# Kernel tuning notes

Hardware: AMD Instinct MI355X
Metric: run time of the kernel (lower is better)

The kernel has to match this reference:

```python
import jax, jax.numpy as jnp
import numpy as np

DIM = 1024; HEADS = 16; HEAD_DIM = 64; LAYERS = 6
P = 2; IMG = 64; CIN = 4; NUM_CLASSES = 1000
CONV_C = DIM // 2  # 512
FF = 2816  # multiple_of-rounded int(2*4*DIM/3)
GN_GROUPS = 32
BATCH = 4


def _layernorm(x, g=None, b=None, eps=1e-5):
    mu = x.mean(-1, keepdims=True)
    var = x.var(-1, keepdims=True)
    xn = (x - mu) / jnp.sqrt(var + eps)
    if g is not None:
        xn = xn * g + b
    return xn


def _groupnorm(x, g, b, eps=1e-5):
    Bn, C, H, W = x.shape
    xr = x.reshape(Bn, GN_GROUPS, C // GN_GROUPS, H, W)
    mu = xr.mean((2, 3, 4), keepdims=True)
    var = xr.var((2, 3, 4), keepdims=True)
    xn = ((xr - mu) / jnp.sqrt(var + eps)).reshape(Bn, C, H, W)
    return xn * g[None, :, None, None] + b[None, :, None, None]


def _conv(x, w, b):
    y = jax.lax.conv_general_dilated(x, w, (1, 1), 'SAME',
                                     dimension_numbers=('NCHW', 'OIHW', 'NCHW'))
    return y + b[None, :, None, None]


def _freqs(T):
    inv = 1.0 / (10000.0 ** (jnp.arange(0, HEAD_DIM, 2, dtype=jnp.float32) / HEAD_DIM))
    f = jnp.arange(T, dtype=jnp.float32)[:, None] * inv[None, :]
    return jnp.stack([jnp.cos(f), jnp.sin(f)], axis=-1)  # [T, HEAD_DIM//2, 2]


def _rope(x, fc):
    # x: [B, T, H, D]; fc: [T, D//2, 2]
    xr = x.reshape(*x.shape[:-1], -1, 2)
    x0, x1 = xr[..., 0], xr[..., 1]
    f0 = fc[None, :, None, :, 0]
    f1 = fc[None, :, None, :, 1]
    y = jnp.stack([x0 * f0 - x1 * f1, x0 * f1 + x1 * f0], axis=-1)
    return y.reshape(x.shape)


def _modulate(x, shift, scale):
    return x * (1.0 + scale[:, None, :]) + shift[:, None, :]


def _forward(x, t, conv1_w, conv1_b, gn1_g, gn1_b, conv2_w, conv2_b, gn2_g, gn2_b,
             xemb_w, xemb_b, t1_w, t1_b, t2_w, t2_b, y_emb,
             wq, wk, wv, wo, w1, w2, w3, ada_w, ada_b, an_g, an_b, fn_g, fn_b,
             fin_ada_w, fin_ada_b, fin_w, fin_b, y):
    # init conv stack: Conv-SiLU-GN x2
    h = _conv(x, conv1_w, conv1_b)
    h = _groupnorm(jax.nn.silu(h), gn1_g, gn1_b)
    h = _conv(h, conv2_w, conv2_b)
    h = _groupnorm(jax.nn.silu(h), gn2_g, gn2_b)
    # patchify: [B,C,H,W] -> [B, N, C*P*P]
    Bn, C, H, W = h.shape
    hp, wp = H // P, W // P
    h = h.reshape(Bn, C, hp, P, wp, P).transpose(0, 2, 4, 1, 3, 5).reshape(Bn, hp * wp, C * P * P)
    z = h @ xemb_w.T + xemb_b  # [B, N, DIM]
    # conditioning: timestep MLP + class embedding
    temb = t.reshape(-1, 1) @ t1_w.T + t1_b
    temb = jax.nn.silu(temb) @ t2_w.T + t2_b
    c = temb + y_emb[y]  # [B, DIM]
    c_silu = jax.nn.silu(c)
    T = z.shape[1]
    fc = _freqs(T)
    scale = HEAD_DIM ** -0.5
    for i in range(LAYERS):
        mods = c_silu @ ada_w[i].T + ada_b[i]
        sm, scm, gm, sp, scp, gp = jnp.split(mods, 6, axis=1)
        hh = _modulate(_layernorm(z, an_g[i], an_b[i]), sm, scm)
        q = (hh @ wq[i].T).reshape(Bn, T, HEADS, HEAD_DIM)
        k = (hh @ wk[i].T).reshape(Bn, T, HEADS, HEAD_DIM)
        v = (hh @ wv[i].T).reshape(Bn, T, HEADS, HEAD_DIM)
        q = _rope(q, fc)
        k = _rope(k, fc)
        scores = jnp.einsum('bthd,bshd->bhts', q, k) * scale
        attn = jax.nn.softmax(scores, axis=-1)
        out = jnp.einsum('bhts,bshd->bthd', attn, v).reshape(Bn, T, DIM)
        z = z + gm[:, None, :] * (out @ wo[i].T)
        hf = _modulate(_layernorm(z, fn_g[i], fn_b[i]), sp, scp)
        ff = (jax.nn.silu(hf @ w1[i].T) * (hf @ w3[i].T)) @ w2[i].T
        z = z + gp[:, None, :] * ff
    # final layer (norm has no affine, eps=1e-6)
    fm = c_silu @ fin_ada_w.T + fin_ada_b
    fs, fsc = jnp.split(fm, 2, axis=1)
    zf = _modulate(_layernorm(z, eps=1e-6), fs, fsc)
    o = zf @ fin_w.T + fin_b  # [B, N, P*P*CIN]
    # unpatchify -> [B, CIN, IMG, IMG]
    o = o.reshape(Bn, hp, wp, P, P, CIN).transpose(0, 5, 1, 3, 2, 4).reshape(Bn, CIN, hp * P, wp * P)
    return o


def setup_inputs() -> dict:
    ks = iter(jax.random.split(jax.random.key(0), 64))

    def nrm(shape, s=0.02):
        return jax.random.normal(next(ks), shape, jnp.float32) * s

    inp = {
        'x': jax.random.normal(next(ks), (BATCH, CIN, IMG, IMG), jnp.float32),
        't': jax.random.uniform(next(ks), (BATCH,), jnp.float32),
        'y': jax.random.randint(next(ks), (BATCH,), 0, NUM_CLASSES + 1),
        'conv1_w': nrm((CONV_C, CIN, 5, 5)), 'conv1_b': jnp.zeros((CONV_C,), jnp.float32),
        'gn1_g': jnp.ones((CONV_C,), jnp.float32), 'gn1_b': jnp.zeros((CONV_C,), jnp.float32),
        'conv2_w': nrm((CONV_C, CONV_C, 5, 5)), 'conv2_b': jnp.zeros((CONV_C,), jnp.float32),
        'gn2_g': jnp.ones((CONV_C,), jnp.float32), 'gn2_b': jnp.zeros((CONV_C,), jnp.float32),
        'xemb_w': nrm((DIM, P * P * CONV_C)), 'xemb_b': jnp.zeros((DIM,), jnp.float32),
        't1_w': nrm((DIM, 1)), 't1_b': jnp.zeros((DIM,), jnp.float32),
        't2_w': nrm((DIM, DIM)), 't2_b': jnp.zeros((DIM,), jnp.float32),
        'y_emb': nrm((NUM_CLASSES + 1, DIM)),
        'wq': nrm((LAYERS, DIM, DIM)), 'wk': nrm((LAYERS, DIM, DIM)),
        'wv': nrm((LAYERS, DIM, DIM)), 'wo': nrm((LAYERS, DIM, DIM)),
        'w1': nrm((LAYERS, FF, DIM)), 'w3': nrm((LAYERS, FF, DIM)), 'w2': nrm((LAYERS, DIM, FF)),
        'ada_w': nrm((LAYERS, 6 * DIM, DIM)), 'ada_b': jnp.zeros((LAYERS, 6 * DIM), jnp.float32),
        'an_g': jnp.ones((LAYERS, DIM), jnp.float32), 'an_b': jnp.zeros((LAYERS, DIM), jnp.float32),
        'fn_g': jnp.ones((LAYERS, DIM), jnp.float32), 'fn_b': jnp.zeros((LAYERS, DIM), jnp.float32),
        'fin_ada_w': nrm((2 * DIM, DIM)), 'fin_ada_b': jnp.zeros((2 * DIM,), jnp.float32),
        'fin_w': nrm((P * P * CIN, DIM)), 'fin_b': jnp.zeros((P * P * CIN,), jnp.float32),
    }
    return inp


def reference(x, t, y, conv1_w, conv1_b, gn1_g, gn1_b, conv2_w, conv2_b, gn2_g, gn2_b,
              xemb_w, xemb_b, t1_w, t1_b, t2_w, t2_b, y_emb,
              wq, wk, wv, wo, w1, w2, w3, ada_w, ada_b, an_g, an_b, fn_g, fn_b,
              fin_ada_w, fin_ada_b, fin_w, fin_b):
    return _forward(x, t, conv1_w, conv1_b, gn1_g, gn1_b, conv2_w, conv2_b, gn2_g, gn2_b,
                    xemb_w, xemb_b, t1_w, t1_b, t2_w, t2_b, y_emb,
                    wq, wk, wv, wo, w1, w2, w3, ada_w, ada_b, an_g, an_b, fn_g, fn_b,
                    fin_ada_w, fin_ada_b, fin_w, fin_b, y)
```

## Files before the change

### kernel.cpp

```cpp
#include <hip/hip_runtime.h>
#include <math.h>

#define NLAYERS 6

typedef unsigned short u16;
typedef unsigned int u32;
typedef __attribute__((ext_vector_type(4))) float floatx4;
typedef __attribute__((ext_vector_type(8))) short bf16x8;

__device__ __forceinline__ float silu_f(float x) { return x / (1.0f + __expf(-x)); }

__device__ __forceinline__ u16 f2b(float f) {
    union { float f; u32 u; } x; x.f = f;
    u32 r = x.u + 0x7fffu + ((x.u >> 16) & 1u);
    return (u16)(r >> 16);
}
__device__ __forceinline__ float b2f(u16 u) {
    union { u32 u; float f; } x; x.u = ((u32)u) << 16;
    return x.f;
}

__device__ __forceinline__ void gload_lds16(const void* g, void* l) {
    __builtin_amdgcn_global_load_lds((const __attribute__((address_space(1))) u32*)g,
                                     (__attribute__((address_space(3))) u32*)l, 16, 0, 0);
}

__device__ __forceinline__ void stage128x32(const u16* __restrict__ src, int ldk, short* lds, int t) {
    int w = t >> 6;
#pragma unroll
    for (int rep = 0; rep < 2; rep++) {
        int s = rep * 256 + t;
        int row = s >> 2, kp = s & 3;
        const u16* g = src + (size_t)row * ldk + kp * 8;
        short* lb = lds + (size_t)(rep * 256 + w * 64) * 8;
        gload_lds16((const void*)g, (void*)lb);
    }
}

__device__ __forceinline__ void stage_attn128x64(const u16* __restrict__ base, short* lds, int t) {
    int w = t >> 6;
#pragma unroll
    for (int rep = 0; rep < 4; rep++) {
        int cid = rep * 256 + t;
        int row = cid >> 3, cc = cid & 7;
        int gcc = cc ^ (row & 7);
        const u16* g = base + (size_t)row * 1024 + gcc * 8;
        short* lb = lds + (size_t)(rep * 256 + w * 64) * 8;
        gload_lds16((const void*)g, (void*)lb);
    }
}

__device__ __forceinline__ void stage_attn64x128(const u16* __restrict__ base, short* lds, int t) {
    int w = t >> 6;
#pragma unroll
    for (int rep = 0; rep < 4; rep++) {
        int cid = rep * 256 + t;
        int row = cid >> 4, cc = cid & 15;
        int gcc = (cc & 8) | ((cc ^ row) & 7);
        const u16* g = base + (size_t)row * 1024 + gcc * 8;
        short* lb = lds + (size_t)(rep * 256 + w * 64) * 8;
        gload_lds16((const void*)g, (void*)lb);
    }
}

__global__ __launch_bounds__(256) void mfma_gemm_kernel(
    const u16* __restrict__ A, const u16* __restrict__ W, int M, int N, int K,
    float* __restrict__ outF, u16* __restrict__ outB, const float* __restrict__ bias,
    float* __restrict__ accZ, const float* __restrict__ gate, int gateStride) {
    __shared__ __align__(16) short As[128 * 32];
    __shared__ __align__(16) short Bs[128 * 32];
    int t = threadIdx.x;
    int lane = t & 63, wave = t >> 6;
    int wm = wave >> 1, wn = wave & 1;
    int m0 = blockIdx.y << 7, n0 = blockIdx.x << 7;
    int lm = lane & 15, kg = lane >> 4;
    floatx4 zero4 = {0.f, 0.f, 0.f, 0.f};
    floatx4 acc[4][4];
#pragma unroll
    for (int i = 0; i < 4; i++)
#pragma unroll
        for (int j = 0; j < 4; j++) acc[i][j] = zero4;
    const u16* Arow = A + (size_t)m0 * K;
    const u16* Wrow = W + (size_t)n0 * K;
    int aoff[4], boff[4];
#pragma unroll
    for (int i = 0; i < 4; i++) {
        aoff[i] = (wm * 64 + i * 16 + lm) * 32 + kg * 8;
        boff[i] = (wn * 64 + i * 16 + lm) * 32 + kg * 8;
    }
    for (int k0 = 0; k0 < K; k0 += 32) {
        stage128x32(Arow + k0, K, As, t);
        stage128x32(Wrow + k0, K, Bs, t);
        __syncthreads();
        bf16x8 af[4], bfr[4];
#pragma unroll
        for (int i = 0; i < 4; i++) af[i] = *(const bf16x8*)&As[aoff[i]];
#pragma unroll
        for (int j = 0; j < 4; j++) bfr[j] = *(const bf16x8*)&Bs[boff[j]];
#pragma unroll
        for (int i = 0; i < 4; i++)
#pragma unroll
            for (int j = 0; j < 4; j++)
                acc[i][j] = __builtin_amdgcn_mfma_f32_16x16x32_bf16(af[i], bfr[j], acc[i][j], 0, 0, 0);
        __syncthreads();
    }
#pragma unroll
    for (int i = 0; i < 4; i++) {
        int rbase = m0 + wm * 64 + i * 16 + kg * 4;
#pragma unroll
        for (int j = 0; j < 4; j++) {
            int c = n0 + wn * 64 + j * 16 + lm;
#pragma unroll
            for (int r = 0; r < 4; r++) {
                float v = acc[i][j][r];
                int row = rbase + r;
                size_t off = (size_t)row * N + c;
                if (accZ) {
                    accZ[off] += gate[(row >> 10) * gateStride + c] * v;
                } else if (outB) {
                    outB[off] = f2b(v);
                } else {
                    if (bias) v += bias[c];
                    outF[off] = v;
                }
            }
        }
    }
}

__global__ __launch_bounds__(256) void mfma_gemm_swiglu_kernel(
    const u16* __restrict__ A, const u16* __restrict__ W1, const u16* __restrict__ W3,
    int M, int N, int K, u16* __restrict__ outB) {
    __shared__ __align__(16) short As[128 * 32];
    __shared__ __align__(16) short B1s[128 * 32];
    __shared__ __align__(16) short B3s[128 * 32];
    int t = threadIdx.x;
    int lane = t & 63, wave = t >> 6;
    int wm = wave >> 1, wn = wave & 1;
    int m0 = blockIdx.y << 7, n0 = blockIdx.x << 7;
    int lm = lane & 15, kg = lane >> 4;
    floatx4 zero4 = {0.f, 0.f, 0.f, 0.f};
    floatx4 acc1[4][4], acc3[4][4];
#pragma unroll
    for (int i = 0; i < 4; i++)
#pragma unroll
        for (int j = 0; j < 4; j++) { acc1[i][j] = zero4; acc3[i][j] = zero4; }
    const u16* Arow = A + (size_t)m0 * K;
    const u16* W1row = W1 + (size_t)n0 * K;
    const u16* W3row = W3 + (size_t)n0 * K;
    int aoff[4], boff[4];
#pragma unroll
    for (int i = 0; i < 4; i++) {
        aoff[i] = (wm * 64 + i * 16 + lm) * 32 + kg * 8;
        boff[i] = (wn * 64 + i * 16 + lm) * 32 + kg * 8;
    }
    for (int k0 = 0; k0 < K; k0 += 32) {
        stage128x32(Arow + k0, K, As, t);
        stage128x32(W1row + k0, K, B1s, t);
        stage128x32(W3row + k0, K, B3s, t);
        __syncthreads();
        bf16x8 af[4], b1[4], b3[4];
#pragma unroll
        for (int i = 0; i < 4; i++) af[i] = *(const bf16x8*)&As[aoff[i]];
#pragma unroll
        for (int j = 0; j < 4; j++) { b1[j] = *(const bf16x8*)&B1s[boff[j]]; b3[j] = *(const bf16x8*)&B3s[boff[j]]; }
#pragma unroll
        for (int i = 0; i < 4; i++)
#pragma unroll
            for (int j = 0; j < 4; j++) {
                acc1[i][j] = __builtin_amdgcn_mfma_f32_16x16x32_bf16(af[i], b1[j], acc1[i][j], 0, 0, 0);
                acc3[i][j] = __builtin_amdgcn_mfma_f32_16x16x32_bf16(af[i], b3[j], acc3[i][j], 0, 0, 0);
            }
        __syncthreads();
    }
#pragma unroll
    for (int i = 0; i < 4; i++) {
        int rbase = m0 + wm * 64 + i * 16 + kg * 4;
#pragma unroll
        for (int j = 0; j < 4; j++) {
            int c = n0 + wn * 64 + j * 16 + lm;
#pragma unroll
            for (int r = 0; r < 4; r++) {
                int row = rbase + r;
                float v = silu_f(acc1[i][j][r]) * acc3[i][j][r];
                outB[(size_t)row * N + c] = f2b(v);
            }
        }
    }
}

__global__ void f2bN_kernel(const float* __restrict__ p0, const float* __restrict__ p1,
                            const float* __restrict__ p2, const float* __restrict__ p3,
                            u16* __restrict__ out, int n4each, int nptr) {
    int idx = blockIdx.x * 256 + threadIdx.x;
    if (idx >= n4each * nptr) return;
    int which = idx / n4each;
    int i = idx - which * n4each;
    const float* p = (which == 0) ? p0 : (which == 1) ? p1 : (which == 2) ? p2 : p3;
    float4 v = ((const float4*)p)[i];
    ushort4 o;
    o.x = f2b(v.x); o.y = f2b(v.y); o.z = f2b(v.z); o.w = f2b(v.w);
    ((ushort4*)out)[idx] = o;
}

__global__ void temb1_kernel(const float* __restrict__ t, const float* __restrict__ w,
                             const float* __restrict__ b, float* __restrict__ out) {
    int idx = blockIdx.x * 256 + threadIdx.x;
    int bb = idx >> 10, n = idx & 1023;
    out[idx] = silu_f(t[bb] * w[n] + b[n]);
}

__global__ __launch_bounds__(256) void temb2_kernel(const float* __restrict__ A, const float* __restrict__ W,
                                                    const float* __restrict__ b2, const float* __restrict__ yemb,
                                                    const int* __restrict__ y, float* __restrict__ out) {
    int wid = blockIdx.x * 4 + (threadIdx.x >> 6);
    int lane = threadIdx.x & 63;
    int bb = wid >> 10, n = wid & 1023;
    const float* a = A + (bb << 10);
    const float* w = W + (n << 10);
    float s = 0.f;
    for (int k = lane << 2; k < 1024; k += 256) {
        float4 av = *(const float4*)&a[k];
        float4 wv = *(const float4*)&w[k];
        s += av.x * wv.x + av.y * wv.y + av.z * wv.z + av.w * wv.w;
    }
#pragma unroll
    for (int off = 32; off > 0; off >>= 1) s += __shfl_xor(s, off);
    if (lane == 0) {
        float vv = s + b2[n] + yemb[(size_t)y[bb] * 1024 + n];
        out[wid] = silu_f(vv);
    }
}

__global__ __launch_bounds__(256) void conv1_kernel(const float* __restrict__ x, const float* __restrict__ w,
                                                    const float* __restrict__ bias, float* __restrict__ out) {
    int idx = blockIdx.x * 256 + threadIdx.x;
    int px = idx & 63;
    int py = (idx >> 6) & 63;
    int oc = (idx >> 12) & 511;
    int b = idx >> 21;
    float acc = bias[oc];
    for (int ic = 0; ic < 4; ic++) {
        const float* xp = x + (((b << 2) + ic) << 12);
        const float* wp = w + (oc * 4 + ic) * 25;
#pragma unroll
        for (int ky = 0; ky < 5; ky++) {
            int iy = py + ky - 2;
            if (iy < 0 || iy > 63) continue;
#pragma unroll
            for (int kx = 0; kx < 5; kx++) {
                int ix = px + kx - 2;
                if (ix < 0 || ix > 63) continue;
                acc += xp[(iy << 6) + ix] * wp[ky * 5 + kx];
            }
        }
    }
    out[idx] = acc;
}

__global__ __launch_bounds__(256) void silu_gn_kernel(const float* __restrict__ in, float* __restrict__ out,
                                                      const float* __restrict__ g, const float* __restrict__ bt) {
    int blk = blockIdx.x;
    int b = blk >> 5, grp = blk & 31, c0 = grp << 4;
    const float* p = in + (size_t)((b * 512 + c0)) * 4096;
    float* q = out + (size_t)((b * 512 + c0)) * 4096;
    int t = threadIdx.x;
    float s = 0.f, sq = 0.f;
    for (int i = t; i < 16384; i += 256) {
        float4 v = ((const float4*)p)[i];
        float a0 = silu_f(v.x), a1 = silu_f(v.y), a2 = silu_f(v.z), a3 = silu_f(v.w);
        s += a0 + a1 + a2 + a3;
        sq += a0 * a0 + a1 * a1 + a2 * a2 + a3 * a3;
    }
    __shared__ float2 red[256];
    red[t] = make_float2(s, sq);
    __syncthreads();
    for (int st = 128; st > 0; st >>= 1) {
        if (t < st) { red[t].x += red[t + st].x; red[t].y += red[t + st].y; }
        __syncthreads();
    }
    float mean = red[0].x * (1.f / 65536.f);
    float var = red[0].y * (1.f / 65536.f) - mean * mean;
    float rstd = rsqrtf(var + 1e-5f);
    for (int i = t; i < 16384; i += 256) {
        float4 v = ((const float4*)p)[i];
        int ch = c0 + (i >> 10);
        float gg = g[ch], bb = bt[ch];
        float4 o;
        o.x = (silu_f(v.x) - mean) * rstd * gg + bb;
        o.y = (silu_f(v.y) - mean) * rstd * gg + bb;
        o.z = (silu_f(v.z) - mean) * rstd * gg + bb;
        o.w = (silu_f(v.w) - mean) * rstd * gg + bb;
        ((float4*)q)[i] = o;
    }
}

__global__ __launch_bounds__(256) void nchw2nhwc_pad_kernel(const float* __restrict__ in, u16* __restrict__ out) {
    int blk = blockIdx.x;
    int ct = blk & 15;
    int yy = (blk >> 4) & 63;
    int b = blk >> 10;
    __shared__ float tile[32][65];
    int t = threadIdx.x;
    const float* ip = in + (((size_t)(b * 512 + (ct << 5))) << 12) + (yy << 6);
    for (int i = t; i < 2048; i += 256) {
        int cl = i >> 6, x = i & 63;
        tile[cl][x] = ip[((size_t)cl << 12) + x];
    }
    __syncthreads();
    u16* op = out + ((size_t)((b * 68 + yy + 2) * 68 + 2)) * 512 + (ct << 5);
    for (int i = t; i < 2048; i += 256) {
        int x = i >> 5, cl = i & 31;
        op[(size_t)x * 512 + cl] = f2b(tile[cl][x]);
    }
}

__global__ __launch_bounds__(256) void wtrans25_kernel(const float* __restrict__ w, u16* __restrict__ wt) {
    int idx = blockIdx.x * 256 + threadIdx.x;
    const float* p = w + (size_t)idx * 25;
#pragma unroll
    for (int tap = 0; tap < 25; tap++)
        wt[(size_t)tap * 262144 + idx] = f2b(p[tap]);
}

__global__ __launch_bounds__(256) void conv2_mfma_kernel(
    const u16* __restrict__ Ipad, const u16* __restrict__ Wt,
    const float* __restrict__ bias, float* __restrict__ out) {
    __shared__ __align__(16) short As[128 * 32];
    __shared__ __align__(16) short Bs[128 * 32];
    int t = threadIdx.x;
    int lane = t & 63, wave = t >> 6;
    int wm = wave >> 1, wn = wave & 1;
    int m0 = blockIdx.y << 7;
    int b = blockIdx.x >> 5;
    int y0 = (blockIdx.x & 31) << 1;
    int lm = lane & 15, kg = lane >> 4;
    floatx4 zero4 = {0.f, 0.f, 0.f, 0.f};
    floatx4 acc[4][4];
#pragma unroll
    for (int i = 0; i < 4; i++)
#pragma unroll
        for (int j = 0; j < 4; j++) acc[i][j] = zero4;
    int aoff[4], boff[4];
#pragma unroll
    for (int i = 0; i < 4; i++) {
        aoff[i] = (wm * 64 + i * 16 + lm) * 32 + kg * 8;
        boff[i] = (wn * 64 + i * 16 + lm) * 32 + kg * 8;
    }
    int s0 = t, s1 = 256 + t;
    int row0 = s0 >> 2, kp0 = s0 & 3;
    int row1 = s1 >> 2, kp1 = s1 & 3;
    int po0 = (row0 >> 6) * 68 + (row0 & 63);
    int po1 = (row1 >> 6) * 68 + (row1 & 63);
    short* lb0 = Bs + (size_t)(wave * 64) * 8;
    short* lb1 = Bs + (size_t)(256 + wave * 64) * 8;
    const u16* ibase = Ipad + ((size_t)(b * 68 + y0) * 68) * 512;
    int tap = 0;
    for (int ky = 0; ky < 5; ky++) {
        for (int kx = 0; kx < 5; kx++, tap++) {
            const u16* wsrc = Wt + (size_t)tap * 262144 + (size_t)m0 * 512;
            const u16* isrc = ibase + (size_t)(ky * 68 + kx) * 512;
            const u16* g0 = isrc + (size_t)po0 * 512 + kp0 * 8;
            const u16* g1 = isrc + (size_t)po1 * 512 + kp1 * 8;
            for (int k0 = 0; k0 < 512; k0 += 32) {
                stage128x32(wsrc + k0, 512, As, t);
                gload_lds16((const void*)(g0 + k0), (void*)lb0);
                gload_lds16((const void*)(g1 + k0), (void*)lb1);
                __syncthreads();
                bf16x8 af[4], bfr[4];
#pragma unroll
                for (int i = 0; i < 4; i++) af[i] = *(const bf16x8*)&As[aoff[i]];
#pragma unroll
                for (int j = 0; j < 4; j++) bfr[j] = *(const bf16x8*)&Bs[boff[j]];
#pragma unroll
                for (int i = 0; i < 4; i++)
#pragma unroll
                    for (int j = 0; j < 4; j++)
                        acc[i][j] = __builtin_amdgcn_mfma_f32_16x16x32_bf16(af[i], bfr[j], acc[i][j], 0, 0, 0);
                __syncthreads();
            }
        }
    }
#pragma unroll
    for (int i = 0; i < 4; i++) {
        int ocbase = m0 + wm * 64 + i * 16 + kg * 4;
#pragma unroll
        for (int j = 0; j < 4; j++) {
            int c = wn * 64 + j * 16 + lm;
            int py = y0 + (c >> 6), px = c & 63;
#pragma unroll
            for (int r = 0; r < 4; r++) {
                int oc = ocbase + r;
                out[((size_t)(b * 512 + oc) << 12) + (py << 6) + px] = acc[i][j][r] + bias[oc];
            }
        }
    }
}

__global__ void patchify_kernel(const float* __restrict__ hn, u16* __restrict__ pout) {
    int idx = blockIdx.x * 256 + threadIdx.x;
    int kf = idx & 2047;
    int tk = (idx >> 11) & 1023;
    int b = idx >> 21;
    int c = kf >> 2;
    int a = (kf >> 1) & 1;
    int b2 = kf & 1;
    int ph = tk >> 5, pw = tk & 31;
    pout[idx] = f2b(hn[(size_t)((b * 512 + c)) * 4096 + (((ph << 1) + a) << 6) + (pw << 1) + b2]);
}

template <typename OT>
__global__ __launch_bounds__(256) void ln_mod_kernel(const float* __restrict__ in, OT* __restrict__ out,
                                                     const float* __restrict__ g, const float* __restrict__ bt,
                                                     const float* __restrict__ shiftb, const float* __restrict__ scaleb,
                                                     int modStride, float eps) {
    int row = blockIdx.x;
    int b = row >> 10;
    int t = threadIdx.x;
    const float* p = in + ((size_t)row << 10);
    float4 x = ((const float4*)p)[t];
    float s = x.x + x.y + x.z + x.w;
    float sq = x.x * x.x + x.y * x.y + x.z * x.z + x.w * x.w;
    __shared__ float2 red[256];
    red[t] = make_float2(s, sq);
    __syncthreads();
    for (int st = 128; st > 0; st >>= 1) {
        if (t < st) { red[t].x += red[t + st].x; red[t].y += red[t + st].y; }
        __syncthreads();
    }
    float mean = red[0].x * (1.f / 1024.f);
    float var = red[0].y * (1.f / 1024.f) - mean * mean;
    float rstd = rsqrtf(var + eps);
    const float* sh = shiftb + b * modStride;
    const float* sc = scaleb + b * modStride;
    int c = t << 2;
    float o0, o1, o2, o3;
    {
        float xn = (x.x - mean) * rstd; if (g) xn = xn * g[c + 0] + bt[c + 0];
        o0 = xn * (1.f + sc[c + 0]) + sh[c + 0];
    }
    {
        float xn = (x.y - mean) * rstd; if (g) xn = xn * g[c + 1] + bt[c + 1];
        o1 = xn * (1.f + sc[c + 1]) + sh[c + 1];
    }
    {
        float xn = (x.z - mean) * rstd; if (g) xn = xn * g[c + 2] + bt[c + 2];
        o2 = xn * (1.f + sc[c + 2]) + sh[c + 2];
    }
    {
        float xn = (x.w - mean) * rstd; if (g) xn = xn * g[c + 3] + bt[c + 3];
        o3 = xn * (1.f + sc[c + 3]) + sh[c + 3];
    }
    if constexpr (sizeof(OT) == 4) {
        float4 o = make_float4(o0, o1, o2, o3);
        ((float4*)(out + ((size_t)row << 10)))[t] = o;
    } else {
        ushort4 o;
        o.x = f2b(o0); o.y = f2b(o1); o.z = f2b(o2); o.w = f2b(o3);
        ((ushort4*)(out + ((size_t)row << 10)))[t] = o;
    }
}

__global__ void rope_table_kernel(float* __restrict__ RT) {
    int idx = blockIdx.x * 256 + threadIdx.x;
    int j = idx & 31;
    int tt = idx >> 5;
    float inv = powf(10000.f, -(float)j * (1.f / 32.f));
    float ang = (float)tt * inv;
    ((float2*)RT)[idx] = make_float2(cosf(ang), sinf(ang));
}

__global__ void rope_kernel(u16* __restrict__ p, const float* __restrict__ RT) {
    int idx = blockIdx.x * 256 + threadIdx.x;
    int j = idx & 31;
    int tt = (idx >> 9) & 1023;
    float2 cssn = ((const float2*)RT)[(tt << 5) + j];
    float cs = cssn.x, sn = cssn.y;
    int h = (idx >> 5) & 15;
    int b = idx >> 19;
    size_t base = (size_t)(((b << 10) + tt)) * 1024 + (h << 6) + (j << 1);
    ushort2 v = *(ushort2*)&p[base];
    float x = b2f(v.x), yv = b2f(v.y);
    ushort2 o;
    o.x = f2b(x * cs - yv * sn);
    o.y = f2b(x * sn + yv * cs);
    *(ushort2*)&p[base] = o;
}

__global__ __launch_bounds__(256) void vtrans_kernel(const u16* __restrict__ v, u16* __restrict__ vT) {
    int st = blockIdx.x, h = blockIdx.y, b = blockIdx.z;
    int s0 = st << 6;
    __shared__ u16 tile[64][68];
    int t = threadIdx.x;
#pragma unroll
    for (int rep = 0; rep < 4; rep++) {
        int i = rep * 256 + t;
        int sl = i >> 4, d4 = (i & 15) << 2;
        *(ushort4*)&tile[sl][d4] =
            *(const ushort4*)&v[(size_t)((b << 10) + s0 + sl) * 1024 + (h << 6) + d4];
    }
    __syncthreads();
#pragma unroll
    for (int rep = 0; rep < 4; rep++) {
        int i = rep * 256 + t;
        int d = i >> 4, sl4 = (i & 15) << 2;
        ushort4 o;
        o.x = tile[sl4 + 0][d];
        o.y = tile[sl4 + 1][d];
        o.z = tile[sl4 + 2][d];
        o.w = tile[sl4 + 3][d];
        *(ushort4*)&vT[(size_t)(((b * 16 + h) << 6) + d) * 1024 + s0 + sl4] = o;
    }
}

__global__ __launch_bounds__(256, 2) void attn_mfma_kernel(
    const u16* __restrict__ q, const u16* __restrict__ k,
    const u16* __restrict__ vT, u16* __restrict__ o) {
    __shared__ __align__(16) short Ks[128 * 64];
    __shared__ __align__(16) short Vts[64 * 128];
    __shared__ __align__(16) short Ps[4 * 32 * 128];
    int t = threadIdx.x;
    int lane = t & 63, wm = t >> 6;
    int lm = lane & 15, kg = lane >> 4;
    int tq0 = blockIdx.x << 7, h = blockIdx.y, b = blockIdx.z;

    const u16* qbase = q + ((size_t)((b << 10) + tq0 + wm * 32)) * 1024 + (h << 6);
    bf16x8 afq[2][2];
#pragma unroll
    for (int i = 0; i < 2; i++)
#pragma unroll
        for (int kk = 0; kk < 2; kk++)
            afq[i][kk] = *(const bf16x8*)(qbase + (size_t)(i * 16 + lm) * 1024 + kk * 32 + kg * 8);

    floatx4 zero4 = {0.f, 0.f, 0.f, 0.f};
    floatx4 oacc[2][4];
    float m_[2][4], l_[2][4];
#pragma unroll
    for (int i = 0; i < 2; i++)
#pragma unroll
        for (int r = 0; r < 4; r++) { m_[i][r] = -3.0e38f; l_[i][r] = 0.f; }
#pragma unroll
    for (int i = 0; i < 2; i++)
#pragma unroll
        for (int jn = 0; jn < 4; jn++) oacc[i][jn] = zero4;

    const u16* kb0 = k + ((size_t)(b << 10)) * 1024 + (h << 6);
    const u16* vb0 = vT + ((size_t)((b * 16 + h) << 6)) * 1024;
    u16* Pw = (u16*)Ps + wm * 4096;

    for (int s0 = 0; s0 < 1024; s0 += 128) {
        stage_attn128x64(kb0 + (size_t)s0 * 1024, Ks, t);
        stage_attn64x128(vb0 + s0, Vts, t);
        __syncthreads();

        floatx4 sacc[2][8];
#pragma unroll
        for (int i = 0; i < 2; i++)
#pragma unroll
            for (int j = 0; j < 8; j++) sacc[i][j] = zero4;
#pragma unroll
        for (int j = 0; j < 8; j++) {
            int row = j * 16 + lm;
            bf16x8 bk0 = *(const bf16x8*)&Ks[row * 64 + ((kg ^ (row & 7)) << 3)];
            bf16x8 bk1 = *(const bf16x8*)&Ks[row * 64 + (((4 + kg) ^ (row & 7)) << 3)];
#pragma unroll
            for (int i = 0; i < 2; i++) {
                sacc[i][j] = __builtin_amdgcn_mfma_f32_16x16x32_bf16(afq[i][0], bk0, sacc[i][j], 0, 0, 0);
                sacc[i][j] = __builtin_amdgcn_mfma_f32_16x16x32_bf16(afq[i][1], bk1, sacc[i][j], 0, 0, 0);
            }
        }

        float al[2][4], ps[2][4];
#pragma unroll
        for (int i = 0; i < 2; i++)
#pragma unroll
            for (int r = 0; r < 4; r++) {
                float v = sacc[i][0][r];
#pragma unroll
                for (int j = 1; j < 8; j++) v = fmaxf(v, sacc[i][j][r]);
                v = fmaxf(v, __shfl_xor(v, 1));
                v = fmaxf(v, __shfl_xor(v, 2));
                v = fmaxf(v, __shfl_xor(v, 4));
                v = fmaxf(v, __shfl_xor(v, 8));
                float mn = fmaxf(m_[i][r], v * 0.125f);
                al[i][r] = __expf(m_[i][r] - mn);
                m_[i][r] = mn;
                l_[i][r] *= al[i][r];
                ps[i][r] = 0.f;
            }
#pragma unroll
        for (int i = 0; i < 2; i++)
#pragma unroll
            for (int jn = 0; jn < 4; jn++)
#pragma unroll
                for (int r = 0; r < 4; r++) oacc[i][jn][r] *= al[i][r];

#pragma unroll
        for (int i = 0; i < 2; i++)
#pragma unroll
            for (int j = 0; j < 8; j++) {
                int s = j * 16 + lm;
                int chunk = s >> 3;
#pragma unroll
                for (int r = 0; r < 4; r++) {
                    int qr = i * 16 + kg * 4 + r;
                    float e = __expf(fmaf(sacc[i][j][r], 0.125f, -m_[i][r]));
                    ps[i][r] += e;
                    int cs = (chunk & 8) | ((chunk ^ qr) & 7);
                    Pw[qr * 128 + cs * 8 + (s & 7)] = f2b(e);
                }
            }
#pragma unroll
        for (int i = 0; i < 2; i++)
#pragma unroll
            for (int r = 0; r < 4; r++) {
                float v = ps[i][r];
                v += __shfl_xor(v, 1);
                v += __shfl_xor(v, 2);
                v += __shfl_xor(v, 4);
                v += __shfl_xor(v, 8);
                l_[i][r] += v;
            }

#pragma unroll
        for (int ks = 0; ks < 4; ks++) {
            int chunk = ks * 4 + kg;
            bf16x8 pa[2];
#pragma unroll
            for (int i = 0; i < 2; i++) {
                int qr = i * 16 + lm;
                int cs = (chunk & 8) | ((chunk ^ qr) & 7);
                pa[i] = *(const bf16x8*)&Pw[qr * 128 + cs * 8];
            }
#pragma unroll
            for (int jn = 0; jn < 4; jn++) {
                int row = jn * 16 + lm;
                int cs = (chunk & 8) | ((chunk ^ row) & 7);
                bf16x8 bv = *(const bf16x8*)&Vts[row * 128 + cs * 8];
#pragma unroll
                for (int i = 0; i < 2; i++)
                    oacc[i][jn] = __builtin_amdgcn_mfma_f32_16x16x32_bf16(pa[i], bv, oacc[i][jn], 0, 0, 0);
            }
        }
        __syncthreads();
    }

    u16* obase = o + ((size_t)((b << 10) + tq0 + wm * 32)) * 1024 + (h << 6);
#pragma unroll
    for (int i = 0; i < 2; i++)
#pragma unroll
        for (int r = 0; r < 4; r++) {
            float inv = 1.f / l_[i][r];
            int qr = i * 16 + kg * 4 + r;
#pragma unroll
            for (int jn = 0; jn < 4; jn++)
                obase[(size_t)qr * 1024 + jn * 16 + lm] = f2b(oacc[i][jn][r] * inv);
        }
}

__global__ __launch_bounds__(256) void rowvec_gemm_kernel(const float* __restrict__ A, const float* __restrict__ W,
                                                          const float* __restrict__ bias, float* __restrict__ out,
                                                          int N, int K) {
    int wid = blockIdx.x * 4 + (threadIdx.x >> 6);
    int lane = threadIdx.x & 63;
    int b = wid / N, n = wid - b * N;
    const float* a = A + (size_t)b * K;
    const float* w = W + (size_t)n * K;
    float s = 0.f;
    for (int k = lane << 2; k < K; k += 256) {
        float4 av = *(const float4*)&a[k];
        float4 wv = *(const float4*)&w[k];
        s += av.x * wv.x + av.y * wv.y + av.z * wv.z + av.w * wv.w;
    }
#pragma unroll
    for (int off = 32; off > 0; off >>= 1) s += __shfl_xor(s, off);
    if (lane == 0) out[wid] = s + (bias ? bias[n] : 0.f);
}

__global__ __launch_bounds__(256) void fin_gemm_kernel(const float* __restrict__ zf, const float* __restrict__ w,
                                                       const float* __restrict__ bias, float* __restrict__ out) {
    int idx = blockIdx.x * 256 + threadIdx.x;
    int m = idx >> 4, n = idx & 15;
    const float* a = zf + ((size_t)m << 10);
    const float* wp = w + ((size_t)n << 10);
    float s = 0.f;
    for (int k = 0; k < 1024; k += 4) {
        float4 av = *(const float4*)&a[k];
        float4 wv = *(const float4*)&wp[k];
        s += av.x * wv.x + av.y * wv.y + av.z * wv.z + av.w * wv.w;
    }
    out[idx] = s + bias[n];
}

__global__ void unpatch_kernel(const float* __restrict__ ot, float* __restrict__ out) {
    int idx = blockIdx.x * 256 + threadIdx.x;
    int x = idx & 63;
    int yy = (idx >> 6) & 63;
    int ci = (idx >> 12) & 3;
    int b = idx >> 14;
    out[idx] = ot[(size_t)(((b << 10) + ((yy >> 1) << 5) + (x >> 1))) * 16 + (((yy & 1) << 1) + (x & 1)) * 4 + ci];
}

extern "C" void kernel_launch(void* const* d_in, const int* in_sizes, int n_in,
                              void* d_out, int out_size, void* d_ws, size_t ws_size,
                              hipStream_t stream) {
    const float* x       = (const float*)d_in[0];
    const float* tin     = (const float*)d_in[1];
    const int*   y       = (const int*)d_in[2];
    const float* conv1_w = (const float*)d_in[3];
    const float* conv1_b = (const float*)d_in[4];
    const float* gn1_g   = (const float*)d_in[5];
    const float* gn1_b   = (const float*)d_in[6];
    const float* conv2_w = (const float*)d_in[7];
    const float* conv2_b = (const float*)d_in[8];
    const float* gn2_g   = (const float*)d_in[9];
    const float* gn2_b   = (const float*)d_in[10];
    const float* xemb_w  = (const float*)d_in[11];
    const float* xemb_b  = (const float*)d_in[12];
    const float* t1_w    = (const float*)d_in[13];
    const float* t1_b    = (const float*)d_in[14];
    const float* t2_w    = (const float*)d_in[15];
    const float* t2_b    = (const float*)d_in[16];
    const float* y_emb   = (const float*)d_in[17];
    const float* wq      = (const float*)d_in[18];
    const float* wk      = (const float*)d_in[19];
    const float* wv      = (const float*)d_in[20];
    const float* wo      = (const float*)d_in[21];
    const float* w1      = (const float*)d_in[22];
    const float* w3      = (const float*)d_in[23];
    const float* w2      = (const float*)d_in[24];
    const float* ada_w   = (const float*)d_in[25];
    const float* ada_b   = (const float*)d_in[26];
    const float* an_g    = (const float*)d_in[27];
    const float* an_b    = (const float*)d_in[28];
    const float* fn_g    = (const float*)d_in[29];
    const float* fn_b    = (const float*)d_in[30];
    const float* fin_ada_w = (const float*)d_in[31];
    const float* fin_ada_b = (const float*)d_in[32];
    const float* fin_w   = (const float*)d_in[33];
    const float* fin_b   = (const float*)d_in[34];

    char* wsb = (char*)d_ws;
    float* Z    = (float*)(wsb + 0);
    u16*  Wbf   = (u16*)(wsb + (16ull << 20));
    u16*  HHb   = (u16*)(wsb + (34ull << 20));
    u16*  Qb    = (u16*)(wsb + (42ull << 20));
    u16*  Kb    = (u16*)(wsb + (50ull << 20));
    u16*  Vb    = (u16*)(wsb + (58ull << 20));
    u16*  VTb   = (u16*)(wsb + (66ull << 20));
    u16*  AOb   = (u16*)(wsb + (74ull << 20));
    u16*  F1b   = (u16*)(wsb + (82ull << 20));
    float* A0f  = (float*)(wsb + (42ull << 20));
    float* A1f  = (float*)(wsb + (76ull << 20));
    u16*  IPad  = (u16*)(wsb + 0);
    u16*  WTc   = (u16*)(wsb + (20ull << 20));
    u16*  PATb  = (u16*)(wsb + (16ull << 20));
    u16*  XWb   = (u16*)(wsb + (34ull << 20));
    float* ZF   = (float*)(wsb + (42ull << 20));
    float* SM   = (float*)(wsb + (110ull << 20));
    float* TMB  = SM;
    float* CSI  = TMB + 4096;
    float* MODS = CSI + 4096;
    float* FM   = MODS + 24576;
    float* OT   = FM + 8192;
    float* RT   = (float*)(wsb + (112ull << 20));

    hipMemsetAsync(IPad, 0, (size_t)4 * 68 * 68 * 512 * 2, stream);
    rope_table_kernel<<<128, 256, 0, stream>>>(RT);
    wtrans25_kernel<<<1024, 256, 0, stream>>>(conv2_w, WTc);

    temb1_kernel<<<16, 256, 0, stream>>>(tin, t1_w, t1_b, TMB);
    temb2_kernel<<<1024, 256, 0, stream>>>(TMB, t2_w, t2_b, y_emb, y, CSI);

    conv1_kernel<<<32768, 256, 0, stream>>>(x, conv1_w, conv1_b, A0f);
    silu_gn_kernel<<<128, 256, 0, stream>>>(A0f, A1f, gn1_g, gn1_b);
    nchw2nhwc_pad_kernel<<<4096, 256, 0, stream>>>(A1f, IPad);
    conv2_mfma_kernel<<<dim3(128, 4), 256, 0, stream>>>(IPad, WTc, conv2_b, A0f);
    silu_gn_kernel<<<128, 256, 0, stream>>>(A0f, A1f, gn2_g, gn2_b);
    patchify_kernel<<<32768, 256, 0, stream>>>(A1f, PATb);
    f2bN_kernel<<<2048, 256, 0, stream>>>(xemb_w, nullptr, nullptr, nullptr, XWb, 524288, 1);
    mfma_gemm_kernel<<<dim3(8, 32), 256, 0, stream>>>(PATb, XWb, 4096, 1024, 2048,
                                                      Z, nullptr, xemb_b, nullptr, nullptr, 0);

    for (int i = 0; i < NLAYERS; i++) {
        const float* wq_i = wq + (size_t)i * 1048576;
        const float* wk_i = wk + (size_t)i * 1048576;
        const float* wv_i = wv + (size_t)i * 1048576;
        const float* wo_i = wo + (size_t)i * 1048576;
        const float* w1_i = w1 + (size_t)i * 2883584;
        const float* w3_i = w3 + (size_t)i * 2883584;
        const float* w2_i = w2 + (size_t)i * 2883584;
        const float* ada_w_i = ada_w + (size_t)i * 6291456;
        const float* ada_b_i = ada_b + (size_t)i * 6144;

        f2bN_kernel<<<4096, 256, 0, stream>>>(wq_i, wk_i, wv_i, wo_i, Wbf, 262144, 4);
        rowvec_gemm_kernel<<<6144, 256, 0, stream>>>(CSI, ada_w_i, ada_b_i, MODS, 6144, 1024);
        ln_mod_kernel<u16><<<4096, 256, 0, stream>>>(Z, HHb, an_g + i * 1024, an_b + i * 1024,
                                                     MODS + 0, MODS + 1024, 6144, 1e-5f);
        mfma_gemm_kernel<<<dim3(8, 32), 256, 0, stream>>>(HHb, Wbf + 0ull, 4096, 1024, 1024,
                                                          nullptr, Qb, nullptr, nullptr, nullptr, 0);
        mfma_gemm_kernel<<<dim3(8, 32), 256, 0, stream>>>(HHb, Wbf + 1048576ull, 4096, 1024, 1024,
                                                          nullptr, Kb, nullptr, nullptr, nullptr, 0);
        mfma_gemm_kernel<<<dim3(8, 32), 256, 0, stream>>>(HHb, Wbf + 2097152ull, 4096, 1024, 1024,
                                                          nullptr, Vb, nullptr, nullptr, nullptr, 0);
        rope_kernel<<<8192, 256, 0, stream>>>(Qb, RT);
        rope_kernel<<<8192, 256, 0, stream>>>(Kb, RT);
        vtrans_kernel<<<dim3(16, 16, 4), 256, 0, stream>>>(Vb, VTb);
        attn_mfma_kernel<<<dim3(8, 16, 4), 256, 0, stream>>>(Qb, Kb, VTb, AOb);
        mfma_gemm_kernel<<<dim3(8, 32), 256, 0, stream>>>(AOb, Wbf + 3145728ull, 4096, 1024, 1024,
                                                          nullptr, nullptr, nullptr, Z, MODS + 2048, 6144);
        ln_mod_kernel<u16><<<4096, 256, 0, stream>>>(Z, HHb, fn_g + i * 1024, fn_b + i * 1024,
                                                     MODS + 3072, MODS + 4096, 6144, 1e-5f);
        f2bN_kernel<<<8448, 256, 0, stream>>>(w1_i, w3_i, w2_i, nullptr, Wbf, 720896, 3);
        mfma_gemm_swiglu_kernel<<<dim3(22, 32), 256, 0, stream>>>(HHb, Wbf, Wbf + 2883584ull,
                                                                  4096, 2816, 1024, F1b);
        mfma_gemm_kernel<<<dim3(8, 32), 256, 0, stream>>>(F1b, Wbf + 5767168ull, 4096, 1024, 2816,
                                                          nullptr, nullptr, nullptr, Z, MODS + 5120, 6144);
    }

    rowvec_gemm_kernel<<<2048, 256, 0, stream>>>(CSI, fin_ada_w, fin_ada_b, FM, 2048, 1024);
    ln_mod_kernel<float><<<4096, 256, 0, stream>>>(Z, ZF, nullptr, nullptr, FM + 0, FM + 1024, 2048, 1e-6f);
    fin_gemm_kernel<<<256, 256, 0, stream>>>(ZF, fin_w, fin_b, OT);
    unpatch_kernel<<<256, 256, 0, stream>>>(OT, (float*)d_out);
}
```

Measured before the change: 3.882 ms.

## Fuse QKV GEMMs with RoPE, add 128x64 GEMM tiles, prioritize attention MFMAs

Q, K and V projections now run as one GEMM over the concatenated weight (N=3072), and the epilogue applies RoPE using lane shuffles, so the three separate launches and two rope passes go away. N=1024 GEMMs (x-embed, output projection, FFN down) switch to a 128x64 tile kernel that launches 512 blocks instead of 256, which should fill the MI355X's many CUs better. The attention kernel raises wave priority with s_setprio around its MFMA loops. The trade-off is less reuse per block with the smaller tiles, and an extra RT table lookup in the QKV epilogue.

Result: faster. 3.463 ms (-10.8%).

```diff
diff --git a/kernel.cpp b/kernel.cpp
--- a/kernel.cpp
+++ b/kernel.cpp
@@ -35,6 +35,14 @@
         short* lb = lds + (size_t)(rep * 256 + w * 64) * 8;
         gload_lds16((const void*)g, (void*)lb);
     }
+}
+
+__device__ __forceinline__ void stage64x32(const u16* __restrict__ src, int ldk, short* lds, int t) {
+    int w = t >> 6;
+    int row = t >> 2, kp = t & 3;
+    const u16* g = src + (size_t)row * ldk + kp * 8;
+    short* lb = lds + (size_t)(w * 64) * 8;
+    gload_lds16((const void*)g, (void*)lb);
 }
 
 __device__ __forceinline__ void stage_attn128x64(const u16* __restrict__ base, short* lds, int t) {
@@ -63,10 +71,10 @@
     }
 }
 
-__global__ __launch_bounds__(256) void mfma_gemm_kernel(
-    const u16* __restrict__ A, const u16* __restrict__ W, int M, int N, int K,
-    float* __restrict__ outF, u16* __restrict__ outB, const float* __restrict__ bias,
-    float* __restrict__ accZ, const float* __restrict__ gate, int gateStride) {
+__global__ __launch_bounds__(256) void mfma_qkv_kernel(
+    const u16* __restrict__ A, const u16* __restrict__ W, const float* __restrict__ RT,
+    u16* __restrict__ Qb, u16* __restrict__ Kb, u16* __restrict__ Vb) {
+    const int K = 1024;
     __shared__ __align__(16) short As[128 * 32];
     __shared__ __align__(16) short Bs[128 * 32];
     int t = threadIdx.x;
@@ -110,6 +118,73 @@
 #pragma unroll
         for (int j = 0; j < 4; j++) {
             int c = n0 + wn * 64 + j * 16 + lm;
+            int which = c >> 10, cc = c & 1023;
+            u16* outp = (which == 0) ? Qb : (which == 1) ? Kb : Vb;
+            int fi = (cc >> 1) & 31;
+#pragma unroll
+            for (int r = 0; r < 4; r++) {
+                int row = rbase + r;
+                float v = acc[i][j][r];
+                float pv = __shfl_xor(v, 1);
+                float res = v;
+                if (which < 2) {
+                    int tt = row & 1023;
+                    float2 cssn = ((const float2*)RT)[(tt << 5) + fi];
+                    res = (lane & 1) ? fmaf(pv, cssn.y, v * cssn.x)
+                                     : fmaf(v, cssn.x, -pv * cssn.y);
+                }
+                outp[(size_t)row * 1024 + cc] = f2b(res);
+            }
+        }
+    }
+}
+
+__global__ __launch_bounds__(256) void mfma_gemm64_kernel(
+    const u16* __restrict__ A, const u16* __restrict__ W, int M, int N, int K,
+    float* __restrict__ outF, const float* __restrict__ bias,
+    float* __restrict__ accZ, const float* __restrict__ gate, int gateStride) {
+    __shared__ __align__(16) short As[128 * 32];
+    __shared__ __align__(16) short Bs[64 * 32];
+    int t = threadIdx.x;
+    int lane = t & 63, wave = t >> 6;
+    int wm = wave >> 1, wn = wave & 1;
+    int m0 = blockIdx.y << 7, n0 = blockIdx.x << 6;
+    int lm = lane & 15, kg = lane >> 4;
+    floatx4 zero4 = {0.f, 0.f, 0.f, 0.f};
+    floatx4 acc[4][2];
+#pragma unroll
+    for (int i = 0; i < 4; i++)
+#pragma unroll
+        for (int j = 0; j < 2; j++) acc[i][j] = zero4;
+    const u16* Arow = A + (size_t)m0 * K;
+    const u16* Wrow = W + (size_t)n0 * K;
+    int aoff[4], boff[2];
+#pragma unroll
+    for (int i = 0; i < 4; i++) aoff[i] = (wm * 64 + i * 16 + lm) * 32 + kg * 8;
+#pragma unroll
+    for (int j = 0; j < 2; j++) boff[j] = (wn * 32 + j * 16 + lm) * 32 + kg * 8;
+    for (int k0 = 0; k0 < K; k0 += 32) {
+        stage128x32(Arow + k0, K, As, t);
+        stage64x32(Wrow + k0, K, Bs, t);
+        __syncthreads();
+        bf16x8 af[4], bfr[2];
+#pragma unroll
+        for (int i = 0; i < 4; i++) af[i] = *(const bf16x8*)&As[aoff[i]];
+#pragma unroll
+        for (int j = 0; j < 2; j++) bfr[j] = *(const bf16x8*)&Bs[boff[j]];
+#pragma unroll
+        for (int i = 0; i < 4; i++)
+#pragma unroll
+            for (int j = 0; j < 2; j++)
+                acc[i][j] = __builtin_amdgcn_mfma_f32_16x16x32_bf16(af[i], bfr[j], acc[i][j], 0, 0, 0);
+        __syncthreads();
+    }
+#pragma unroll
+    for (int i = 0; i < 4; i++) {
+        int rbase = m0 + wm * 64 + i * 16 + kg * 4;
+#pragma unroll
+        for (int j = 0; j < 2; j++) {
+            int c = n0 + wn * 32 + j * 16 + lm;
 #pragma unroll
             for (int r = 0; r < 4; r++) {
                 float v = acc[i][j][r];
@@ -117,8 +192,6 @@
                 size_t off = (size_t)row * N + c;
                 if (accZ) {
                     accZ[off] += gate[(row >> 10) * gateStride + c] * v;
-                } else if (outB) {
-                    outB[off] = f2b(v);
                 } else {
                     if (bias) v += bias[c];
                     outF[off] = v;
@@ -470,23 +543,6 @@
     ((float2*)RT)[idx] = make_float2(cosf(ang), sinf(ang));
 }
 
-__global__ void rope_kernel(u16* __restrict__ p, const float* __restrict__ RT) {
-    int idx = blockIdx.x * 256 + threadIdx.x;
-    int j = idx & 31;
-    int tt = (idx >> 9) & 1023;
-    float2 cssn = ((const float2*)RT)[(tt << 5) + j];
-    float cs = cssn.x, sn = cssn.y;
-    int h = (idx >> 5) & 15;
-    int b = idx >> 19;
-    size_t base = (size_t)(((b << 10) + tt)) * 1024 + (h << 6) + (j << 1);
-    ushort2 v = *(ushort2*)&p[base];
-    float x = b2f(v.x), yv = b2f(v.y);
-    ushort2 o;
-    o.x = f2b(x * cs - yv * sn);
-    o.y = f2b(x * sn + yv * cs);
-    *(ushort2*)&p[base] = o;
-}
-
 __global__ __launch_bounds__(256) void vtrans_kernel(const u16* __restrict__ v, u16* __restrict__ vT) {
     int st = blockIdx.x, h = blockIdx.y, b = blockIdx.z;
     int s0 = st << 6;
@@ -558,6 +614,7 @@
         for (int i = 0; i < 2; i++)
 #pragma unroll
             for (int j = 0; j < 8; j++) sacc[i][j] = zero4;
+        __builtin_amdgcn_s_setprio(1);
 #pragma unroll
         for (int j = 0; j < 8; j++) {
             int row = j * 16 + lm;
@@ -569,6 +626,7 @@
                 sacc[i][j] = __builtin_amdgcn_mfma_f32_16x16x32_bf16(afq[i][1], bk1, sacc[i][j], 0, 0, 0);
             }
         }
+        __builtin_amdgcn_s_setprio(0);
 
         float al[2][4], ps[2][4];
 #pragma unroll
@@ -622,6 +680,7 @@
                 l_[i][r] += v;
             }
 
+        __builtin_amdgcn_s_setprio(1);
 #pragma unroll
         for (int ks = 0; ks < 4; ks++) {
             int chunk = ks * 4 + kg;
@@ -642,6 +701,7 @@
                     oacc[i][jn] = __builtin_amdgcn_mfma_f32_16x16x32_bf16(pa[i], bv, oacc[i][jn], 0, 0, 0);
             }
         }
+        __builtin_amdgcn_s_setprio(0);
         __syncthreads();
     }
 
@@ -779,8 +839,8 @@
     silu_gn_kernel<<<128, 256, 0, stream>>>(A0f, A1f, gn2_g, gn2_b);
     patchify_kernel<<<32768, 256, 0, stream>>>(A1f, PATb);
     f2bN_kernel<<<2048, 256, 0, stream>>>(xemb_w, nullptr, nullptr, nullptr, XWb, 524288, 1);
-    mfma_gemm_kernel<<<dim3(8, 32), 256, 0, stream>>>(PATb, XWb, 4096, 1024, 2048,
-                                                      Z, nullptr, xemb_b, nullptr, nullptr, 0);
+    mfma_gemm64_kernel<<<dim3(16, 32), 256, 0, stream>>>(PATb, XWb, 4096, 1024, 2048,
+                                                         Z, xemb_b, nullptr, nullptr, 0);
 
     for (int i = 0; i < NLAYERS; i++) {
         const float* wq_i = wq + (size_t)i * 1048576;
@@ -797,25 +857,18 @@
         rowvec_gemm_kernel<<<6144, 256, 0, stream>>>(CSI, ada_w_i, ada_b_i, MODS, 6144, 1024);
         ln_mod_kernel<u16><<<4096, 256, 0, stream>>>(Z, HHb, an_g + i * 1024, an_b + i * 1024,
                                                      MODS + 0, MODS + 1024, 6144, 1e-5f);
-        mfma_gemm_kernel<<<dim3(8, 32), 256, 0, stream>>>(HHb, Wbf + 0ull, 4096, 1024, 1024,
-                                                          nullptr, Qb, nullptr, nullptr, nullptr, 0);
-        mfma_gemm_kernel<<<dim3(8, 32), 256, 0, stream>>>(HHb, Wbf + 1048576ull, 4096, 1024, 1024,
-                                                          nullptr, Kb, nullptr, nullptr, nullptr, 0);
-        mfma_gemm_kernel<<<dim3(8, 32), 256, 0, stream>>>(HHb, Wbf + 2097152ull, 4096, 1024, 1024,
-                                                          nullptr, Vb, nullptr, nullptr, nullptr, 0);
-        rope_kernel<<<8192, 256, 0, stream>>>(Qb, RT);
-        rope_kernel<<<8192, 256, 0, stream>>>(Kb, RT);
+        mfma_qkv_kernel<<<dim3(24, 32), 256, 0, stream>>>(HHb, Wbf, RT, Qb, Kb, Vb);
         vtrans_kernel<<<dim3(16, 16, 4), 256, 0, stream>>>(Vb, VTb);
         attn_mfma_kernel<<<dim3(8, 16, 4), 256, 0, stream>>>(Qb, Kb, VTb, AOb);
-        mfma_gemm_kernel<<<dim3(8, 32), 256, 0, stream>>>(AOb, Wbf + 3145728ull, 4096, 1024, 1024,
-                                                          nullptr, nullptr, nullptr, Z, MODS + 2048, 6144);
+        mfma_gemm64_kernel<<<dim3(16, 32), 256, 0, stream>>>(AOb, Wbf + 3145728ull, 4096, 1024, 1024,
+                                                             nullptr, nullptr, Z, MODS + 2048, 6144);
         ln_mod_kernel<u16><<<4096, 256, 0, stream>>>(Z, HHb, fn_g + i * 1024, fn_b + i * 1024,
                                                      MODS + 3072, MODS + 4096, 6144, 1e-5f);
         f2bN_kernel<<<8448, 256, 0, stream>>>(w1_i, w3_i, w2_i, nullptr, Wbf, 720896, 3);
         mfma_gemm_swiglu_kernel<<<dim3(22, 32), 256, 0, stream>>>(HHb, Wbf, Wbf + 2883584ull,
                                                                   4096, 2816, 1024, F1b);
-        mfma_gemm_kernel<<<dim3(8, 32), 256, 0, stream>>>(F1b, Wbf + 5767168ull, 4096, 1024, 2816,
-                                                          nullptr, nullptr, nullptr, Z, MODS + 5120, 6144);
+        mfma_gemm64_kernel<<<dim3(16, 32), 256, 0, stream>>>(F1b, Wbf + 5767168ull, 4096, 1024, 2816,
+                                                             nullptr, nullptr, Z, MODS + 5120, 6144);
     }
 
     rowvec_gemm_kernel<<<2048, 256, 0, stream>>>(CSI, fin_ada_w, fin_ada_b, FM, 2048, 1024);
```
